# Optimization experiments

Hardware: AMD Instinct MI355X
Metric: run time of the kernel (lower is better)

Reference implementation:

```python
import jax, jax.numpy as jnp
import numpy as np

N = 8192
DIN = 256
DOUT = 128
ALPHA = 0.2      # leaky-relu negative slope
K_MAX = 32       # static upper bound on action.max()+1 (action in [0, 32))
NEG_BIG = -9.0e15


def setup_inputs() -> dict:
    key = jax.random.key(0)
    ks = jax.random.split(key, 6)
    xavier_w = 1.414 * np.sqrt(6.0 / (DIN + DOUT))
    xavier_a = 1.414 * np.sqrt(6.0 / (DOUT + 1))
    return {
        "input": jax.random.normal(ks[0], (N, DIN), dtype=jnp.float32),
        "adj": jax.random.randint(ks[1], (N, N), 0, 2, dtype=jnp.int32),
        "action": jax.random.randint(ks[2], (N,), 0, K_MAX, dtype=jnp.int32),
        "W": jax.random.uniform(ks[3], (DIN, DOUT), jnp.float32, -xavier_w, xavier_w),
        "a_self": jax.random.uniform(ks[4], (DOUT, 1), jnp.float32, -xavier_a, xavier_a),
        "a_neighs": jax.random.uniform(ks[5], (DOUT, 1), jnp.float32, -xavier_a, xavier_a),
        "breadth_policy": 1,
    }


def reference(input, adj, action, W, a_self, a_neighs, breadth_policy):
    h = input @ W                                  # [N, DOUT]
    attn_self = h @ a_self                         # [N, 1]
    attn_neighs = h @ a_neighs                     # [N, 1]
    e = jax.nn.leaky_relu(attn_self + attn_neighs.T, negative_slope=ALPHA)  # [N, N]
    masked = jnp.where(adj > 0, e, jnp.float32(NEG_BIG))
    attention = jax.nn.softmax(masked, axis=1)     # [N, N]
    if breadth_policy:
        # static K_MAX >= action.max()+1; thresholds only read index action[i]
        top_vals, _ = jax.lax.top_k(attention, K_MAX)          # [N, K_MAX], sorted desc
        thresholds = top_vals[jnp.arange(N), action]           # [N]
        attention = jnp.where(attention < thresholds[:, None], 0.0, attention)
    h_prime = attention @ h                        # [N, DOUT]
    return jax.nn.elu(h_prime)                     # concat=True
```

## Files before the change

kernel.cpp:

```cpp
#include <hip/hip_runtime.h>
#include <cstdint>
#include <cstddef>

#define NN   8192
#define DIN  256
#define DOUT 128
#define LRA  0.2f

__global__ __launch_bounds__(256) void gemm_h_kernel(
    const float* __restrict__ input, const float* __restrict__ W,
    float* __restrict__ h)
{
    __shared__ float tile[16][DIN];
    const int row0 = blockIdx.x * 16;
    {
        const float4* in4 = (const float4*)(input + (size_t)row0 * DIN);
        float4* t4 = (float4*)&tile[0][0];
        for (int k = threadIdx.x; k < 16 * DIN / 4; k += 256) t4[k] = in4[k];
    }
    __syncthreads();
    const int c = threadIdx.x & 127;
    const int g = threadIdx.x >> 7;
    float acc[8] = {0.f, 0.f, 0.f, 0.f, 0.f, 0.f, 0.f, 0.f};
    for (int k = 0; k < DIN; k += 4) {
        const float w0 = W[(k + 0) * DOUT + c];
        const float w1 = W[(k + 1) * DOUT + c];
        const float w2 = W[(k + 2) * DOUT + c];
        const float w3 = W[(k + 3) * DOUT + c];
        #pragma unroll
        for (int m = 0; m < 8; ++m) {
            const float4 av = *(const float4*)&tile[g * 8 + m][k];
            acc[m] += av.x * w0 + av.y * w1 + av.z * w2 + av.w * w3;
        }
    }
    #pragma unroll
    for (int m = 0; m < 8; ++m)
        h[(size_t)(row0 + g * 8 + m) * DOUT + c] = acc[m];
}

__global__ __launch_bounds__(256) void attn_vec_kernel(
    const float* __restrict__ h, const float* __restrict__ a_self,
    const float* __restrict__ a_neighs, float* __restrict__ s,
    float* __restrict__ t)
{
    const int wid  = (blockIdx.x * 256 + threadIdx.x) >> 6;
    const int lane = threadIdx.x & 63;
    if (wid >= NN) return;
    const float h0 = h[(size_t)wid * DOUT + lane];
    const float h1 = h[(size_t)wid * DOUT + 64 + lane];
    float vs = h0 * a_self[lane]   + h1 * a_self[64 + lane];
    float vn = h0 * a_neighs[lane] + h1 * a_neighs[64 + lane];
    for (int off = 32; off > 0; off >>= 1) {
        vs += __shfl_down(vs, off);
        vn += __shfl_down(vn, off);
    }
    if (lane == 0) { s[wid] = vs; t[wid] = vn; }
}

__global__ __launch_bounds__(256) void rank_kernel(
    const float* __restrict__ t, int* __restrict__ order)
{
    __shared__ float tl[NN];
    __shared__ int   part[8][32];
    for (int k = threadIdx.x; k < NN; k += 256) tl[k] = t[k];
    __syncthreads();
    const int jloc = threadIdx.x & 31;
    const int seg  = threadIdx.x >> 5;
    const int j    = blockIdx.x * 32 + jloc;
    const float tj = tl[j];
    int r = 0;
    const int k0 = seg * (NN / 8);
    for (int k = k0; k < k0 + NN / 8; ++k) {
        const float tk = tl[k];
        r += (tk > tj) ? 1 : ((tk == tj && k < j) ? 1 : 0);
    }
    part[seg][jloc] = r;
    __syncthreads();
    if (threadIdx.x < 32) {
        int rr = 0;
        #pragma unroll
        for (int ss = 0; ss < 8; ++ss) rr += part[ss][threadIdx.x];
        order[rr] = blockIdx.x * 32 + threadIdx.x;
    }
}

__global__ __launch_bounds__(256) void gat_row_kernel(
    const int* __restrict__ adj, const float* __restrict__ s_arr,
    const float* __restrict__ t_arr, const int* __restrict__ order,
    const int* __restrict__ action, const float* __restrict__ h,
    const int* __restrict__ policy, float* __restrict__ out)
{
    __shared__ float tl[NN];
    __shared__ float red[256];
    __shared__ float numlds[2][128];
    __shared__ int   sel_j[64];
    __shared__ float sel_w[64];
    __shared__ int   sel_cnt_sh;
    __shared__ int   done_sh;

    const int row = blockIdx.x;
    const int tid = threadIdx.x;
    {
        const float4* t4 = (const float4*)t_arr;
        float4* tl4 = (float4*)tl;
        for (int k = tid; k < NN / 4; k += 256) tl4[k] = t4[k];
    }
    __syncthreads();

    const float s    = s_arr[row];
    const float tmax = tl[order[0]];
    const float zc   = s + tmax;
    const float C    = fmaxf(zc, LRA * zc);

    const int4*   arow = (const int4*)(adj + (size_t)row * NN);
    const float4* tl4c = (const float4*)tl;
    float acc = 0.f;
    #pragma unroll
    for (int k = 0; k < 8; ++k) {
        const int idx = tid + k * 256;
        const int4   a  = arow[idx];
        const float4 tv = tl4c[idx];
        float z, e, w;
        z = s + tv.x; e = fmaxf(z, LRA * z); w = __expf(e - C); if (a.x > 0) acc += w;
        z = s + tv.y; e = fmaxf(z, LRA * z); w = __expf(e - C); if (a.y > 0) acc += w;
        z = s + tv.z; e = fmaxf(z, LRA * z); w = __expf(e - C); if (a.z > 0) acc += w;
        z = s + tv.w; e = fmaxf(z, LRA * z); w = __expf(e - C); if (a.w > 0) acc += w;
    }
    red[tid] = acc;
    __syncthreads();
    for (int off = 128; off > 0; off >>= 1) {
        if (tid < off) red[tid] += red[tid + off];
        __syncthreads();
    }
    const float l = red[0];

    int K = action[row] + 1;
    if (policy[0] == 0) K = 0x7FFFFFFF;
    const int c = tid & 127;
    const int g = tid >> 7;
    float accv = 0.f;

    const int lane = tid & 63;
    float tthr = -3.0e38f;
    int found = 0;
    int cnt = 0;
    int base = 0;

    while (true) {
        if (tid < 64) {
            const int p = base + lane;
            int j = 0, valid = 0;
            float tj = -3.0e38f;
            if (p < NN) {
                j     = order[p];
                tj    = tl[j];
                valid = (adj[(size_t)row * NN + j] > 0) ? 1 : 0;
            }
            const unsigned long long vm = __ballot(valid);
            if (!found) {
                const int cv = __popcll(vm);
                if (cnt + cv >= K) {
                    const int need = K - cnt;
                    const int myrank =
                        __popcll(vm & ((1ull << lane) - 1ull)) + 1;
                    const unsigned long long pm =
                        __ballot(valid && (myrank == need));
                    const int L = __ffsll((long long)pm) - 1;
                    tthr  = __shfl(tj, L);
                    found = 1;
                } else {
                    cnt += cv;
                }
            }
            const int selected = valid && (tj >= tthr);
            const unsigned long long sm = __ballot(selected);
            const int pos = __popcll(sm & ((1ull << lane) - 1ull));
            if (selected) {
                const float z = s + tj;
                const float e = fmaxf(z, LRA * z);
                sel_j[pos] = j;
                sel_w[pos] = __expf(e - C);
            }
            if (lane == 0) {
                sel_cnt_sh = __popcll(sm);
                const int nb = base + 64;
                int dn;
                if (nb >= NN)      dn = 1;
                else if (found)    dn = (tl[order[nb]] < tthr) ? 1 : 0;
                else               dn = 0;
                done_sh = dn;
            }
        }
        __syncthreads();
        const int nsel = sel_cnt_sh;
        const int dn   = done_sh;
        for (int e2 = g; e2 < nsel; e2 += 2)
            accv += sel_w[e2] * h[(size_t)sel_j[e2] * DOUT + c];
        base += 64;
        if (dn) break;
        __syncthreads();
    }

    numlds[g][c] = accv;
    __syncthreads();
    if (tid < 128) {
        const float v = (numlds[0][tid] + numlds[1][tid]) / l;
        out[(size_t)row * DOUT + tid] = (v > 0.f) ? v : expm1f(v);
    }
}

extern "C" void kernel_launch(void* const* d_in, const int* in_sizes, int n_in,
                              void* d_out, int out_size, void* d_ws,
                              size_t ws_size, hipStream_t stream)
{
    const float* input    = (const float*)d_in[0];
    const int*   adj      = (const int*)d_in[1];
    const int*   action   = (const int*)d_in[2];
    const float* W        = (const float*)d_in[3];
    const float* a_self   = (const float*)d_in[4];
    const float* a_neighs = (const float*)d_in[5];
    const int*   policy   = (const int*)d_in[6];
    float* out = (float*)d_out;

    float* ws    = (float*)d_ws;
    float* h     = ws;
    float* s     = ws + (size_t)NN * DOUT;
    float* t     = s + NN;
    int*   order = (int*)(t + NN);

    hipLaunchKernelGGL(gemm_h_kernel, dim3(512), dim3(256), 0, stream,
                       input, W, h);
    hipLaunchKernelGGL(attn_vec_kernel, dim3(2048), dim3(256), 0, stream,
                       h, a_self, a_neighs, s, t);
    hipLaunchKernelGGL(rank_kernel, dim3(256), dim3(256), 0, stream,
                       t, order);
    hipLaunchKernelGGL(gat_row_kernel, dim3(8192), dim3(256), 0, stream,
                       adj, s, t, order, action, h, policy, out);
}
```

Before: 430.1 us.

## Drop full t staging in row kernel, cache top order in LDS, shuffle reduce

The row kernel no longer copies the whole 32 KB t array into shared memory for each row block. It instead caches the first 256 entries of the sorted order and their t values, and reads everything else from global memory. The sum reduction moves from a tree over shared memory with many barriers to wavefront shuffles. The rank kernel now reads with float4 and unrolls its loop, the GEMM loop gets unroll 2, and the gather loop uses two accumulators for more memory-level parallelism. These changes cut LDS footprint and barriers, which should raise occupancy, at the cost of more global/L2 reads of t.

Result: no change. 426.9 us (-0.7%).

```diff
diff --git a/kernel.cpp b/kernel.cpp
--- a/kernel.cpp
+++ b/kernel.cpp
@@ -22,6 +22,7 @@
     const int c = threadIdx.x & 127;
     const int g = threadIdx.x >> 7;
     float acc[8] = {0.f, 0.f, 0.f, 0.f, 0.f, 0.f, 0.f, 0.f};
+    #pragma unroll 2
     for (int k = 0; k < DIN; k += 4) {
         const float w0 = W[(k + 0) * DOUT + c];
         const float w1 = W[(k + 1) * DOUT + c];
@@ -70,9 +71,15 @@
     const float tj = tl[j];
     int r = 0;
     const int k0 = seg * (NN / 8);
-    for (int k = k0; k < k0 + NN / 8; ++k) {
-        const float tk = tl[k];
-        r += (tk > tj) ? 1 : ((tk == tj && k < j) ? 1 : 0);
+    const float4* tl4 = (const float4*)(tl + k0);
+    #pragma unroll 4
+    for (int k = 0; k < NN / 8 / 4; ++k) {
+        const float4 tv = tl4[k];
+        const int kb = k0 + 4 * k;
+        r += (tv.x > tj) ? 1 : ((tv.x == tj && (kb + 0) < j) ? 1 : 0);
+        r += (tv.y > tj) ? 1 : ((tv.y == tj && (kb + 1) < j) ? 1 : 0);
+        r += (tv.z > tj) ? 1 : ((tv.z == tj && (kb + 2) < j) ? 1 : 0);
+        r += (tv.w > tj) ? 1 : ((tv.w == tj && (kb + 3) < j) ? 1 : 0);
     }
     part[seg][jloc] = r;
     __syncthreads();
@@ -90,8 +97,9 @@
     const int* __restrict__ action, const float* __restrict__ h,
     const int* __restrict__ policy, float* __restrict__ out)
 {
-    __shared__ float tl[NN];
-    __shared__ float red[256];
+    __shared__ int   ord_s[256];
+    __shared__ float ts_s[256];
+    __shared__ float red4[4];
     __shared__ float numlds[2][128];
     __shared__ int   sel_j[64];
     __shared__ float sel_w[64];
@@ -100,45 +108,44 @@
 
     const int row = blockIdx.x;
     const int tid = threadIdx.x;
+
     {
-        const float4* t4 = (const float4*)t_arr;
-        float4* tl4 = (float4*)tl;
-        for (int k = tid; k < NN / 4; k += 256) tl4[k] = t4[k];
+        const int oj = order[tid];
+        ord_s[tid] = oj;
+        ts_s[tid]  = t_arr[oj];
     }
     __syncthreads();
 
     const float s    = s_arr[row];
-    const float tmax = tl[order[0]];
+    const float tmax = ts_s[0];
     const float zc   = s + tmax;
     const float C    = fmaxf(zc, LRA * zc);
 
     const int4*   arow = (const int4*)(adj + (size_t)row * NN);
-    const float4* tl4c = (const float4*)tl;
+    const float4* t4   = (const float4*)t_arr;
     float acc = 0.f;
     #pragma unroll
     for (int k = 0; k < 8; ++k) {
         const int idx = tid + k * 256;
         const int4   a  = arow[idx];
-        const float4 tv = tl4c[idx];
+        const float4 tv = t4[idx];
         float z, e, w;
         z = s + tv.x; e = fmaxf(z, LRA * z); w = __expf(e - C); if (a.x > 0) acc += w;
         z = s + tv.y; e = fmaxf(z, LRA * z); w = __expf(e - C); if (a.y > 0) acc += w;
         z = s + tv.z; e = fmaxf(z, LRA * z); w = __expf(e - C); if (a.z > 0) acc += w;
         z = s + tv.w; e = fmaxf(z, LRA * z); w = __expf(e - C); if (a.w > 0) acc += w;
     }
-    red[tid] = acc;
-    __syncthreads();
-    for (int off = 128; off > 0; off >>= 1) {
-        if (tid < off) red[tid] += red[tid + off];
-        __syncthreads();
-    }
-    const float l = red[0];
+    #pragma unroll
+    for (int off = 32; off > 0; off >>= 1) acc += __shfl_down(acc, off);
+    if ((tid & 63) == 0) red4[tid >> 6] = acc;
+    __syncthreads();
+    const float l = red4[0] + red4[1] + red4[2] + red4[3];
 
     int K = action[row] + 1;
     if (policy[0] == 0) K = 0x7FFFFFFF;
     const int c = tid & 127;
     const int g = tid >> 7;
-    float accv = 0.f;
+    float accv = 0.f, accv2 = 0.f;
 
     const int lane = tid & 63;
     float tthr = -3.0e38f;
@@ -152,8 +159,8 @@
             int j = 0, valid = 0;
             float tj = -3.0e38f;
             if (p < NN) {
-                j     = order[p];
-                tj    = tl[j];
+                if (p < 256) { j = ord_s[p]; tj = ts_s[p]; }
+                else         { j = order[p]; tj = t_arr[j]; }
                 valid = (adj[(size_t)row * NN + j] > 0) ? 1 : 0;
             }
             const unsigned long long vm = __ballot(valid);
@@ -185,21 +192,30 @@
                 sel_cnt_sh = __popcll(sm);
                 const int nb = base + 64;
                 int dn;
-                if (nb >= NN)      dn = 1;
-                else if (found)    dn = (tl[order[nb]] < tthr) ? 1 : 0;
-                else               dn = 0;
+                if (nb >= NN) dn = 1;
+                else if (found) {
+                    const float tnb = (nb < 256) ? ts_s[nb] : t_arr[order[nb]];
+                    dn = (tnb < tthr) ? 1 : 0;
+                } else dn = 0;
                 done_sh = dn;
             }
         }
         __syncthreads();
         const int nsel = sel_cnt_sh;
         const int dn   = done_sh;
-        for (int e2 = g; e2 < nsel; e2 += 2)
-            accv += sel_w[e2] * h[(size_t)sel_j[e2] * DOUT + c];
+        for (int e2 = g; e2 < nsel; e2 += 4) {
+            const float w0 = sel_w[e2];
+            const float v0 = h[(size_t)sel_j[e2] * DOUT + c];
+            if (e2 + 2 < nsel) {
+                accv2 += sel_w[e2 + 2] * h[(size_t)sel_j[e2 + 2] * DOUT + c];
+            }
+            accv += w0 * v0;
+        }
         base += 64;
         if (dn) break;
         __syncthreads();
     }
+    accv += accv2;
 
     numlds[g][c] = accv;
     __syncthreads();
```
